# Kernel optimization log

Hardware: AMD Instinct MI355X
Metric: run time of the kernel (lower is better)

## Reference

```python
import jax, jax.numpy as jnp
import numpy as np

K_MASK = -2.3819763e+38
ROPE_THETA = 1000000
MROPE_SECTION = (24, 20, 20)
NORM_EPS = 1e-6


def rms_norm(x, w, eps=NORM_EPS):
    dtype = x.dtype
    x32 = x.astype(jnp.float32)
    rms_inv = jax.lax.rsqrt(jnp.mean(x32 * x32, axis=-1, keepdims=True) + eps)
    return w * (x32 * rms_inv).astype(dtype)


def apply_rope(inputs, positions, head_dim, rope_theta=ROPE_THETA, mrope_section=MROPE_SECTION):
    # positions: [3, B, T] (temporal, height, width); inputs: [B, T, heads, head_dim]
    fraction = 2 * jnp.arange(0, head_dim // 2, dtype=jnp.float32) / head_dim
    timescale = rope_theta ** fraction  # [head_dim//2]
    sinusoid = positions[:, :, :, None].astype(jnp.float32) / timescale  # [3,B,T,hd/2]
    freq = sinusoid[0]
    h_idx = jnp.arange(1, mrope_section[1] * 3, 3)
    w_idx = jnp.arange(2, mrope_section[2] * 3, 3)
    freq = freq.at[..., h_idx].set(sinusoid[1][..., h_idx])
    freq = freq.at[..., w_idx].set(sinusoid[2][..., w_idx])
    freq = freq[:, :, None, :]  # [B,T,1,hd/2]
    sin, cos = jnp.sin(freq), jnp.cos(freq)
    first, second = jnp.split(inputs, 2, axis=-1)
    out = jnp.concatenate([first * cos - second * sin, second * cos + first * sin], axis=-1)
    return out.astype(inputs.dtype)


def setup_inputs() -> dict:
    key = jax.random.key(0)
    ks = jax.random.split(key, 6)
    B, T, D, N, K, H = 2, 1024, 2560, 32, 8, 128
    x = jax.random.normal(ks[0], (B, T, D), dtype=jnp.float32)
    positions = jnp.broadcast_to(jnp.arange(T, dtype=jnp.int32), (3, B, T))
    attn_mask = jnp.tril(jnp.ones((T, T), dtype=bool))[None].repeat(B, axis=0)  # causal [B,T,T]
    wq = jax.random.normal(ks[1], (D, N, H), dtype=jnp.float32) * 0.02
    wk = jax.random.normal(ks[2], (D, K, H), dtype=jnp.float32) * 0.02
    wv = jax.random.normal(ks[3], (D, K, H), dtype=jnp.float32) * 0.02
    wo = jax.random.normal(ks[4], (N, H, D), dtype=jnp.float32) * 0.02
    q_norm_w = jnp.ones((H,), dtype=jnp.float32)
    k_norm_w = jnp.ones((H,), dtype=jnp.float32)
    return {"x": x, "positions": positions, "attn_mask": attn_mask, "wq": wq,
            "wk": wk, "wv": wv, "wo": wo, "q_norm_w": q_norm_w, "k_norm_w": k_norm_w}


def reference(x, positions, attn_mask, wq, wk, wv, wo, q_norm_w, k_norm_w):
    head_dim = wo.shape[1]
    scale = head_dim ** -0.5
    q = rms_norm(jnp.einsum('btd,dnh->btnh', x, wq), q_norm_w)
    k = rms_norm(jnp.einsum('bsd,dkh->bskh', x, wk), k_norm_w)
    v = jnp.einsum('bsd,dkh->bskh', x, wv)
    q = apply_rope(q, positions, head_dim)
    k = apply_rope(k, positions, head_dim)
    b, t, qh, d = q.shape
    _, s, kh, _ = k.shape
    q = q.reshape((b, t, kh, qh // kh, d))  # GQA grouping
    attn = jnp.einsum('bthgd,bshd->bhgts', q, k) * scale
    attn = attn.reshape((b, qh, t, s))
    attn = jnp.where(attn_mask[:, None, :, :], attn, K_MASK)
    attn = jax.nn.softmax(attn.astype(jnp.float32), axis=-1).astype(k.dtype)
    attn = attn.reshape((b, kh, qh // kh, t, s))
    qkv = jnp.einsum('bhgts,bshd->bthgd', attn, v).reshape((b, t, qh, d))
    return jnp.einsum('btnh,nhd->btd', qkv, wo)
```

## Files before the change

kernel.cpp:

```cpp
#include <hip/hip_runtime.h>
#include <hip/hip_bf16.h>

typedef __attribute__((ext_vector_type(8))) __bf16 bf8_t;
typedef __attribute__((ext_vector_type(4))) float f32x4;

#define GLOAD16(gptr, lptr)                                                              \
  __builtin_amdgcn_global_load_lds((const __attribute__((address_space(1))) void*)(gptr), \
                                   (__attribute__((address_space(3))) void*)(lptr), 16, 0, 0)

__device__ __forceinline__ unsigned short f2bf(float f) {
  union { float f; unsigned u; } v; v.f = f;
  return (unsigned short)((v.u + 0x7fffu + ((v.u >> 16) & 1u)) >> 16);
}

__global__ void cast_bf16(const float* __restrict__ in, unsigned short* __restrict__ out, int n4) {
  int i = blockIdx.x * blockDim.x + threadIdx.x;
  if (i >= n4) return;
  float4 v = ((const float4*)in)[i];
  ushort4 o;
  o.x = f2bf(v.x); o.y = f2bf(v.y); o.z = f2bf(v.z); o.w = f2bf(v.w);
  ((ushort4*)out)[i] = o;
}

__global__ void tcast(const float* __restrict__ in, unsigned short* __restrict__ out,
                      int R, int C, int ld, int rowOff) {
  __shared__ float tile[32][33];
  int c0 = blockIdx.x * 32, r0 = blockIdx.y * 32;
  int tx = threadIdx.x, ty = threadIdx.y;
#pragma unroll
  for (int i = 0; i < 4; ++i)
    tile[ty + 8 * i][tx] = in[(size_t)(r0 + ty + 8 * i) * C + c0 + tx];
  __syncthreads();
#pragma unroll
  for (int i = 0; i < 4; ++i)
    out[(size_t)(rowOff + c0 + ty + 8 * i) * ld + r0 + tx] = f2bf(tile[tx][ty + 8 * i]);
}

__global__ __launch_bounds__(512, 2) void gemm256(
    const unsigned short* __restrict__ A,
    const unsigned short* __restrict__ Bt,
    float* __restrict__ C0, float* __restrict__ C1,
    int N, int ldk, int Kslice, int nTileN) {
  __shared__ unsigned short SM[4][2][8192];
  int ks = blockIdx.y;
  float* __restrict__ C = ks ? C1 : C0;
  int kbase = ks * Kslice;
  int bm = blockIdx.x / nTileN, bn = blockIdx.x % nTileN;
  int m0 = bm << 8, n0 = bn << 8;
  int tid = threadIdx.x, lane = tid & 63, w = tid >> 6;
  int wm = w >> 2, wn = w & 3;
  int lrow = lane & 15, lch = lane >> 4;
  int srow = tid >> 2, scol = (tid & 3) << 3;
  int nt = Kslice >> 5;

  f32x4 acc[8][4] = {};

  auto stage = [&](int t) {
    int buf = t & 3;
    int k0 = kbase + (t << 5);
    const unsigned short* Ag = A + (size_t)(m0 + srow) * ldk + k0 + scol;
    const unsigned short* Bg = Bt + (size_t)(n0 + srow) * ldk + k0 + scol;
    unsigned short* Al = &SM[buf][0][w << 9];
    unsigned short* Bl = &SM[buf][1][w << 9];
    GLOAD16(Ag, Al);
    GLOAD16(Ag + (size_t)128 * ldk, Al + 4096);
    GLOAD16(Bg, Bl);
    GLOAD16(Bg + (size_t)128 * ldk, Bl + 4096);
  };

  stage(0);
  stage(1);
  for (int t = 0; t < nt; ++t) {
    if (t + 2 < nt) stage(t + 2);
    if (t + 2 < nt)      asm volatile("s_waitcnt vmcnt(8)" ::: "memory");
    else if (t + 1 < nt) asm volatile("s_waitcnt vmcnt(4)" ::: "memory");
    else                 asm volatile("s_waitcnt vmcnt(0)" ::: "memory");
    asm volatile("s_barrier" ::: "memory");
    int buf = t & 3;
    const unsigned short* As = &SM[buf][0][0];
    const unsigned short* Bs = &SM[buf][1][0];
    bf8_t a[8], b[4];
#pragma unroll
    for (int mi = 0; mi < 8; ++mi)
      a[mi] = *(const bf8_t*)(As + ((wm << 7) + (mi << 4) + lrow) * 32 + (lch << 3));
#pragma unroll
    for (int ni = 0; ni < 4; ++ni)
      b[ni] = *(const bf8_t*)(Bs + ((wn << 6) + (ni << 4) + lrow) * 32 + (lch << 3));
    __builtin_amdgcn_s_setprio(1);
#pragma unroll
    for (int mi = 0; mi < 8; ++mi)
#pragma unroll
      for (int ni = 0; ni < 4; ++ni)
        acc[mi][ni] = __builtin_amdgcn_mfma_f32_16x16x32_bf16(a[mi], b[ni], acc[mi][ni], 0, 0, 0);
    __builtin_amdgcn_s_setprio(0);
  }
  int r0 = m0 + (wm << 7) + (lch << 2);
  int c0 = n0 + (wn << 6) + lrow;
#pragma unroll
  for (int mi = 0; mi < 8; ++mi)
#pragma unroll
    for (int ni = 0; ni < 4; ++ni)
#pragma unroll
      for (int r = 0; r < 4; ++r)
        C[(size_t)(r0 + (mi << 4) + r) * N + c0 + (ni << 4)] = acc[mi][ni][r];
}

__global__ void reduce_add(const float4* __restrict__ a, const float4* __restrict__ b,
                           float4* __restrict__ o, int n4) {
  int i = blockIdx.x * blockDim.x + threadIdx.x;
  if (i >= n4) return;
  float4 x = a[i], y = b[i];
  o[i] = make_float4(x.x + y.x, x.y + y.y, x.z + y.z, x.w + y.w);
}

__global__ __launch_bounds__(128) void normrope(
    const float* __restrict__ qkv, const int* __restrict__ positions,
    const float* __restrict__ qw, const float* __restrict__ kw,
    unsigned short* __restrict__ qb, unsigned short* __restrict__ kb,
    unsigned short* __restrict__ vt) {
  int blk = blockIdx.x;
  int hh = blk % 48, bt = blk / 48;
  int b = bt >> 10, t = bt & 1023;
  int tid = threadIdx.x;
  int colbase = (hh < 32) ? (hh << 7) : ((hh < 40) ? (4096 + ((hh - 32) << 7)) : (5120 + ((hh - 40) << 7)));
  float val = qkv[(size_t)bt * 6144 + colbase + tid];
  if (hh >= 40) {
    vt[((size_t)((b * 8 + hh - 40) * 128 + tid)) * 1024 + t] = f2bf(val);
    return;
  }
  __shared__ float red[2];
  __shared__ float xs[128];
  float ss = val * val;
#pragma unroll
  for (int m = 32; m >= 1; m >>= 1) ss += __shfl_xor(ss, m);
  if ((tid & 63) == 0) red[tid >> 6] = ss;
  __syncthreads();
  float rinv = rsqrtf((red[0] + red[1]) * (1.0f / 128.0f) + 1e-6f);
  float wgt = (hh < 32) ? qw[tid] : kw[tid];
  float xn = val * rinv * wgt;
  xs[tid] = xn;
  __syncthreads();
  float other = xs[tid ^ 64];
  int pos = positions[b * 1024 + t];
  int j = tid & 63;
  float ang = (float)pos * exp2f(-(float)j * 0.31143075889569027f);
  float sv = sinf(ang), cv = cosf(ang);
  float outv = (tid < 64) ? (xn * cv - other * sv) : (xn * cv + other * sv);
  unsigned short o = f2bf(outv);
  if (hh < 32) qb[((size_t)((b * 32 + hh) * 1024 + t)) * 128 + tid] = o;
  else kb[((size_t)((b * 8 + hh - 32) * 1024 + t)) * 128 + tid] = o;
}

__global__ __launch_bounds__(256) void attn(
    const unsigned short* __restrict__ qb,
    const unsigned short* __restrict__ kb,
    const unsigned short* __restrict__ vt,
    unsigned short* __restrict__ ob) {
  __shared__ unsigned short Ks[2][64 * 128];
  __shared__ unsigned short Vs[2][128 * 64];
  __shared__ unsigned short Ps[4][16 * 72];
  int qpair = blockIdx.x, hq = blockIdx.y, b = blockIdx.z;
  int qtA = qpair, qtB = 15 - qpair;
  int kvh = hq >> 2;
  int tid = threadIdx.x, lane = tid & 63, w = tid >> 6;
  int lrow = lane & 15, lko = (lane >> 4) << 3;
  const float scale = 0.08838834764831845f;

  const unsigned short* kbase = kb + ((size_t)(b * 8 + kvh) << 17);
  const unsigned short* vbase = vt + ((size_t)(b * 8 + kvh) << 17);

  int qArow = (qtA << 6) + (w << 4) + lrow;
  int qBrow = (qtB << 6) + (w << 4) + lrow;
  const unsigned short* qpA = qb + ((size_t)((b * 32 + hq) * 1024 + qArow) << 7);
  const unsigned short* qpB = qb + ((size_t)((b * 32 + hq) * 1024 + qBrow) << 7);
  bf8_t qaA[4], qaB[4];
#pragma unroll
  for (int kk = 0; kk < 4; ++kk) {
    qaA[kk] = *(const bf8_t*)(qpA + kk * 32 + lko);
    qaB[kk] = *(const bf8_t*)(qpB + kk * 32 + lko);
  }
  f32x4 accA[8] = {}, accB[8] = {};
  float mA[4], lA[4], mB[4], lB[4];
#pragma unroll
  for (int r = 0; r < 4; ++r) { mA[r] = mB[r] = -3.0e38f; lA[r] = lB[r] = 0.f; }

  int kr_l = lane >> 4, kc_l = lane & 15;
  int vr_l = lane >> 3, vc_l = lane & 7;

  auto stage = [&](int st, int buf) {
    int s0 = st << 6;
    unsigned short* kd = &Ks[buf][0];
    unsigned short* vd = &Vs[buf][0];
#pragma unroll
    for (int i = 0; i < 4; ++i) {
      int si = (w << 2) + i;
      int kr = (si << 2) + kr_l;
      GLOAD16(kbase + (size_t)(s0 + kr) * 128 + ((kc_l ^ (kr & 7)) << 3), kd + (si << 9));
      int vr = (si << 3) + vr_l;
      GLOAD16(vbase + (size_t)vr * 1024 + s0 + ((vc_l ^ (vr & 7)) << 3), vd + (si << 9));
    }
  };

  int qArow0 = (qtA << 6) + (w << 4) + ((lane >> 4) << 2);
  int qBrow0 = (qtB << 6) + (w << 4) + ((lane >> 4) << 2);
  unsigned short* psw = &Ps[w][0];

  auto tilec = [&](int buf, int s0, const bf8_t* qa, f32x4* accO, float* mrun, float* lrun,
                   int qrow0, bool domask) {
    const char* Kb = (const char*)&Ks[buf][0];
    const char* Vb = (const char*)&Vs[buf][0];
    f32x4 sacc[4] = {};
#pragma unroll
    for (int kk = 0; kk < 4; ++kk)
#pragma unroll
      for (int ni = 0; ni < 4; ++ni) {
        int kr = (ni << 4) + lrow;
        const bf8_t* kf = (const bf8_t*)(Kb + kr * 256 + ((((kk << 2) | (lko >> 3)) ^ (kr & 7)) << 4));
        sacc[ni] = __builtin_amdgcn_mfma_f32_16x16x32_bf16(qa[kk], *kf, sacc[ni], 0, 0, 0);
      }
    float p[4][4], rmax[4];
#pragma unroll
    for (int r = 0; r < 4; ++r) rmax[r] = -3.0e38f;
#pragma unroll
    for (int ni = 0; ni < 4; ++ni) {
      int sc = s0 + ni * 16 + lrow;
#pragma unroll
      for (int r = 0; r < 4; ++r) {
        float sv = sacc[ni][r] * scale;
        if (domask) sv = (sc <= qrow0 + r) ? sv : -3.0e38f;
        p[ni][r] = sv;
        rmax[r] = fmaxf(rmax[r], sv);
      }
    }
#pragma unroll
    for (int m = 1; m <= 8; m <<= 1)
#pragma unroll
      for (int r = 0; r < 4; ++r) rmax[r] = fmaxf(rmax[r], __shfl_xor(rmax[r], m));
    float alpha[4], rsum[4];
#pragma unroll
    for (int r = 0; r < 4; ++r) {
      float mn = fmaxf(mrun[r], rmax[r]);
      alpha[r] = __expf(mrun[r] - mn);
      mrun[r] = mn;
      rsum[r] = 0.f;
    }
#pragma unroll
    for (int ni = 0; ni < 4; ++ni)
#pragma unroll
      for (int r = 0; r < 4; ++r) {
        float e = __expf(p[ni][r] - mrun[r]);
        p[ni][r] = e;
        rsum[r] += e;
      }
#pragma unroll
    for (int m = 1; m <= 8; m <<= 1)
#pragma unroll
      for (int r = 0; r < 4; ++r) rsum[r] += __shfl_xor(rsum[r], m);
#pragma unroll
    for (int r = 0; r < 4; ++r) lrun[r] = lrun[r] * alpha[r] + rsum[r];
#pragma unroll
    for (int ni = 0; ni < 8; ++ni)
#pragma unroll
      for (int r = 0; r < 4; ++r) accO[ni][r] *= alpha[r];
#pragma unroll
    for (int ni = 0; ni < 4; ++ni)
#pragma unroll
      for (int r = 0; r < 4; ++r)
        psw[(((lane >> 4) << 2) + r) * 72 + ni * 16 + lrow] = f2bf(p[ni][r]);
    bf8_t pa0 = *(const bf8_t*)(psw + lrow * 72 + lko);
    bf8_t pa1 = *(const bf8_t*)(psw + lrow * 72 + 32 + lko);
#pragma unroll
    for (int ni = 0; ni < 8; ++ni) {
      int vr = (ni << 4) + lrow;
      const bf8_t* v0 = (const bf8_t*)(Vb + vr * 128 + (((lko >> 3) ^ (vr & 7)) << 4));
      const bf8_t* v1 = (const bf8_t*)(Vb + vr * 128 + (((4 | (lko >> 3)) ^ (vr & 7)) << 4));
      accO[ni] = __builtin_amdgcn_mfma_f32_16x16x32_bf16(pa0, *v0, accO[ni], 0, 0, 0);
      accO[ni] = __builtin_amdgcn_mfma_f32_16x16x32_bf16(pa1, *v1, accO[ni], 0, 0, 0);
    }
  };

  stage(0, 0);
  for (int st = 0; st <= qtB; ++st) {
    int buf = st & 1;
    __syncthreads();
    if (st < qtB) stage(st + 1, buf ^ 1);
    if (st <= qtA) tilec(buf, st << 6, qaA, accA, mA, lA, qArow0, st == qtA);
    tilec(buf, st << 6, qaB, accB, mB, lB, qBrow0, st == qtB);
  }

  size_t rowA = (size_t)(b * 1024) + (qtA << 6) + (w << 4) + ((lane >> 4) << 2);
  size_t rowB = (size_t)(b * 1024) + (qtB << 6) + (w << 4) + ((lane >> 4) << 2);
#pragma unroll
  for (int r = 0; r < 4; ++r) {
    float invA = 1.0f / lA[r], invB = 1.0f / lB[r];
#pragma unroll
    for (int ni = 0; ni < 8; ++ni) {
      ob[(rowA + r) * 4096 + hq * 128 + ni * 16 + lrow] = f2bf(accA[ni][r] * invA);
      ob[(rowB + r) * 4096 + hq * 128 + ni * 16 + lrow] = f2bf(accB[ni][r] * invB);
    }
  }
}

extern "C" void kernel_launch(void* const* d_in, const int* in_sizes, int n_in,
                              void* d_out, int out_size, void* d_ws, size_t ws_size,
                              hipStream_t stream) {
  const float* x = (const float*)d_in[0];
  const int* positions = (const int*)d_in[1];
  const float* wq = (const float*)d_in[3];
  const float* wk = (const float*)d_in[4];
  const float* wv = (const float*)d_in[5];
  const float* wo = (const float*)d_in[6];
  const float* qnw = (const float*)d_in[7];
  const float* knw = (const float*)d_in[8];
  float* out = (float*)d_out;

  char* ws = (char*)d_ws;
  unsigned short* x_bf  = (unsigned short*)(ws);
  unsigned short* wqkvT = (unsigned short*)(ws + 10485760);
  unsigned short* woT   = (unsigned short*)(ws + 41943040);
  float*          qkv   = (float*)(ws + 62914560);
  float*          p0    = (float*)(ws + 62914560);
  float*          p1    = (float*)(ws + 83886080);
  unsigned short* q_bf  = (unsigned short*)(ws + 113246208);
  unsigned short* k_bf  = (unsigned short*)(ws + 130023424);
  unsigned short* vt_bf = (unsigned short*)(ws + 134217728);
  unsigned short* a_bf  = (unsigned short*)(ws + 138412032);

  cast_bf16<<<5120, 256, 0, stream>>>(x, x_bf, 2048 * 2560 / 4);
  tcast<<<dim3(128, 80), dim3(32, 8), 0, stream>>>(wq, wqkvT, 2560, 4096, 2560, 0);
  tcast<<<dim3(32, 80), dim3(32, 8), 0, stream>>>(wk, wqkvT, 2560, 1024, 2560, 4096);
  tcast<<<dim3(32, 80), dim3(32, 8), 0, stream>>>(wv, wqkvT, 2560, 1024, 2560, 5120);
  tcast<<<dim3(80, 128), dim3(32, 8), 0, stream>>>(wo, woT, 4096, 2560, 4096, 0);
  gemm256<<<dim3(8 * 24, 1), 512, 0, stream>>>(x_bf, wqkvT, qkv, nullptr, 6144, 2560, 2560, 24);
  normrope<<<2048 * 48, 128, 0, stream>>>(qkv, positions, qnw, knw, q_bf, k_bf, vt_bf);
  attn<<<dim3(8, 32, 2), 256, 0, stream>>>(q_bf, k_bf, vt_bf, a_bf);
  gemm256<<<dim3(8 * 10, 2), 512, 0, stream>>>(a_bf, woT, p0, p1, 2560, 4096, 2048, 10);
  reduce_add<<<5120, 256, 0, stream>>>((const float4*)p0, (const float4*)p1, (float4*)out,
                                       2048 * 2560 / 4);
}
```

Before: 307.6 us.

## Rewrite attention kernel with 32x32 MFMA, 128-row query tiles, register P transpose

```diff
diff --git a/kernel.cpp b/kernel.cpp
--- a/kernel.cpp
+++ b/kernel.cpp
@@ -3,6 +3,7 @@
 
 typedef __attribute__((ext_vector_type(8))) __bf16 bf8_t;
 typedef __attribute__((ext_vector_type(4))) float f32x4;
+typedef __attribute__((ext_vector_type(16))) float f32x16;
 
 #define GLOAD16(gptr, lptr)                                                              \
   __builtin_amdgcn_global_load_lds((const __attribute__((address_space(1))) void*)(gptr), \
@@ -11,6 +12,12 @@
 __device__ __forceinline__ unsigned short f2bf(float f) {
   union { float f; unsigned u; } v; v.f = f;
   return (unsigned short)((v.u + 0x7fffu + ((v.u >> 16) & 1u)) >> 16);
+}
+
+__device__ __forceinline__ unsigned cvtpk_bf16(float a, float b) {
+  unsigned r;
+  asm("v_cvt_pk_bf16_f32 %0, %1, %2" : "=v"(r) : "v"(a), "v"(b));
+  return r;
 }
 
 __global__ void cast_bf16(const float* __restrict__ in, unsigned short* __restrict__ out, int n4) {
@@ -151,153 +158,148 @@
   else kb[((size_t)((b * 8 + hh - 32) * 1024 + t)) * 128 + tid] = o;
 }
 
-__global__ __launch_bounds__(256) void attn(
+__global__ __launch_bounds__(256, 2) void attn(
     const unsigned short* __restrict__ qb,
     const unsigned short* __restrict__ kb,
     const unsigned short* __restrict__ vt,
     unsigned short* __restrict__ ob) {
-  __shared__ unsigned short Ks[2][64 * 128];
-  __shared__ unsigned short Vs[2][128 * 64];
-  __shared__ unsigned short Ps[4][16 * 72];
-  int qpair = blockIdx.x, hq = blockIdx.y, b = blockIdx.z;
-  int qtA = qpair, qtB = 15 - qpair;
+  __shared__ unsigned short Kl[2][64 * 128];
+  __shared__ unsigned short Vl[2][128 * 64];
+  int bx = blockIdx.x, hq = blockIdx.y, b = blockIdx.z;
+  int qt = (bx < 4) ? (7 - bx) : (bx - 4);
   int kvh = hq >> 2;
   int tid = threadIdx.x, lane = tid & 63, w = tid >> 6;
-  int lrow = lane & 15, lko = (lane >> 4) << 3;
-  const float scale = 0.08838834764831845f;
-
+  int qlane = lane & 31, h = lane >> 5;
+  int q0 = (qt << 7) + (w << 5);
+  int qg = q0 + qlane;
   const unsigned short* kbase = kb + ((size_t)(b * 8 + kvh) << 17);
   const unsigned short* vbase = vt + ((size_t)(b * 8 + kvh) << 17);
-
-  int qArow = (qtA << 6) + (w << 4) + lrow;
-  int qBrow = (qtB << 6) + (w << 4) + lrow;
-  const unsigned short* qpA = qb + ((size_t)((b * 32 + hq) * 1024 + qArow) << 7);
-  const unsigned short* qpB = qb + ((size_t)((b * 32 + hq) * 1024 + qBrow) << 7);
-  bf8_t qaA[4], qaB[4];
-#pragma unroll
-  for (int kk = 0; kk < 4; ++kk) {
-    qaA[kk] = *(const bf8_t*)(qpA + kk * 32 + lko);
-    qaB[kk] = *(const bf8_t*)(qpB + kk * 32 + lko);
-  }
-  f32x4 accA[8] = {}, accB[8] = {};
-  float mA[4], lA[4], mB[4], lB[4];
-#pragma unroll
-  for (int r = 0; r < 4; ++r) { mA[r] = mB[r] = -3.0e38f; lA[r] = lB[r] = 0.f; }
-
-  int kr_l = lane >> 4, kc_l = lane & 15;
-  int vr_l = lane >> 3, vc_l = lane & 7;
+  const float c2 = 0.12751744f;
+
+  const unsigned short* qptr = qb + ((size_t)((b * 32 + hq) * 1024 + qg) << 7) + (h << 3);
+  bf8_t qf[8];
+#pragma unroll
+  for (int ds = 0; ds < 8; ++ds) qf[ds] = *(const bf8_t*)(qptr + ds * 16);
+
+  f32x16 o[4] = {};
+  float mrun = -3.0e38f, lrun = 0.f;
+  int last_st = (q0 + 31) >> 6;
+  int nsteps = 2 * qt + 2;
 
   auto stage = [&](int st, int buf) {
     int s0 = st << 6;
-    unsigned short* kd = &Ks[buf][0];
-    unsigned short* vd = &Vs[buf][0];
+    unsigned short* kd = &Kl[buf][0];
+    unsigned short* vd = &Vl[buf][0];
 #pragma unroll
     for (int i = 0; i < 4; ++i) {
-      int si = (w << 2) + i;
-      int kr = (si << 2) + kr_l;
-      GLOAD16(kbase + (size_t)(s0 + kr) * 128 + ((kc_l ^ (kr & 7)) << 3), kd + (si << 9));
-      int vr = (si << 3) + vr_l;
-      GLOAD16(vbase + (size_t)vr * 1024 + s0 + ((vc_l ^ (vr & 7)) << 3), vd + (si << 9));
+      int cid = i * 256 + tid;
+      int kr = cid >> 4, ksl = cid & 15;
+      GLOAD16(kbase + (size_t)(s0 + kr) * 128 + ((ksl ^ (kr & 15)) << 3), kd + cid * 8);
+      int vr = cid >> 3, vsl = cid & 7;
+      GLOAD16(vbase + (size_t)vr * 1024 + s0 + ((vsl ^ (vr & 7)) << 3), vd + cid * 8);
     }
   };
 
-  int qArow0 = (qtA << 6) + (w << 4) + ((lane >> 4) << 2);
-  int qBrow0 = (qtB << 6) + (w << 4) + ((lane >> 4) << 2);
-  unsigned short* psw = &Ps[w][0];
-
-  auto tilec = [&](int buf, int s0, const bf8_t* qa, f32x4* accO, float* mrun, float* lrun,
-                   int qrow0, bool domask) {
-    const char* Kb = (const char*)&Ks[buf][0];
-    const char* Vb = (const char*)&Vs[buf][0];
-    f32x4 sacc[4] = {};
-#pragma unroll
-    for (int kk = 0; kk < 4; ++kk)
-#pragma unroll
-      for (int ni = 0; ni < 4; ++ni) {
-        int kr = (ni << 4) + lrow;
-        const bf8_t* kf = (const bf8_t*)(Kb + kr * 256 + ((((kk << 2) | (lko >> 3)) ^ (kr & 7)) << 4));
-        sacc[ni] = __builtin_amdgcn_mfma_f32_16x16x32_bf16(qa[kk], *kf, sacc[ni], 0, 0, 0);
-      }
-    float p[4][4], rmax[4];
-#pragma unroll
-    for (int r = 0; r < 4; ++r) rmax[r] = -3.0e38f;
-#pragma unroll
-    for (int ni = 0; ni < 4; ++ni) {
-      int sc = s0 + ni * 16 + lrow;
-#pragma unroll
-      for (int r = 0; r < 4; ++r) {
-        float sv = sacc[ni][r] * scale;
-        if (domask) sv = (sc <= qrow0 + r) ? sv : -3.0e38f;
-        p[ni][r] = sv;
-        rmax[r] = fmaxf(rmax[r], sv);
+  stage(0, 0);
+  for (int st = 0; st < nsteps; ++st) {
+    __syncthreads();
+    if (st + 1 < nsteps) stage(st + 1, (st + 1) & 1);
+    if (st <= last_st) {
+      const char* Kb = (const char*)&Kl[st & 1][0];
+      const char* Vb = (const char*)&Vl[st & 1][0];
+      f32x16 s0v = {}, s1v = {};
+#pragma unroll
+      for (int ds = 0; ds < 8; ++ds) {
+        int c = ds * 2 + h;
+        int r0 = qlane, r1 = 32 + qlane;
+        bf8_t k0 = *(const bf8_t*)(Kb + r0 * 256 + ((c ^ (r0 & 15)) << 4));
+        bf8_t k1 = *(const bf8_t*)(Kb + r1 * 256 + ((c ^ (r1 & 15)) << 4));
+        s0v = __builtin_amdgcn_mfma_f32_32x32x16_bf16(k0, qf[ds], s0v, 0, 0, 0);
+        s1v = __builtin_amdgcn_mfma_f32_32x32x16_bf16(k1, qf[ds], s1v, 0, 0, 0);
+      }
+      bool dm = (st == last_st);
+      int kg0 = st << 6;
+      float mt = -3.0e38f;
+#pragma unroll
+      for (int e = 0; e < 16; ++e) {
+        int kl = (e & 3) + 8 * (e >> 2) + 4 * h;
+        if (dm) {
+          if (kg0 + kl > qg) s0v[e] = -3.0e38f;
+          if (kg0 + 32 + kl > qg) s1v[e] = -3.0e38f;
+        }
+        mt = fmaxf(mt, fmaxf(s0v[e], s1v[e]));
+      }
+      mt = fmaxf(mt, __shfl_xor(mt, 32));
+      float mnew = fmaxf(mrun, mt);
+      float alpha = exp2f((mrun - mnew) * c2);
+      float ls = 0.f;
+#pragma unroll
+      for (int e = 0; e < 16; ++e) {
+        s0v[e] = exp2f((s0v[e] - mnew) * c2);
+        s1v[e] = exp2f((s1v[e] - mnew) * c2);
+        ls += s0v[e] + s1v[e];
+      }
+      ls += __shfl_xor(ls, 32);
+      lrun = lrun * alpha + ls;
+      mrun = mnew;
+#pragma unroll
+      for (int db = 0; db < 4; ++db)
+#pragma unroll
+        for (int e = 0; e < 16; ++e) o[db][e] *= alpha;
+      bf8_t pf[4];
+#pragma unroll
+      for (int s = 0; s < 4; ++s) {
+        unsigned w00, w01, w10, w11;
+        {
+          const int B0 = 4 * ((2 * s) & 3);
+          if ((2 * s) >> 2) { w00 = cvtpk_bf16(s1v[B0], s1v[B0 + 1]); w01 = cvtpk_bf16(s1v[B0 + 2], s1v[B0 + 3]); }
+          else              { w00 = cvtpk_bf16(s0v[B0], s0v[B0 + 1]); w01 = cvtpk_bf16(s0v[B0 + 2], s0v[B0 + 3]); }
+        }
+        {
+          const int B1 = 4 * ((2 * s + 1) & 3);
+          if ((2 * s + 1) >> 2) { w10 = cvtpk_bf16(s1v[B1], s1v[B1 + 1]); w11 = cvtpk_bf16(s1v[B1 + 2], s1v[B1 + 3]); }
+          else                  { w10 = cvtpk_bf16(s0v[B1], s0v[B1 + 1]); w11 = cvtpk_bf16(s0v[B1 + 2], s0v[B1 + 3]); }
+        }
+        unsigned sa = h ? w00 : w10, sb = h ? w01 : w11;
+        unsigned ra = __shfl_xor(sa, 32), rb = __shfl_xor(sb, 32);
+        unsigned ka = h ? w10 : w00, kb2 = h ? w11 : w01;
+        unsigned f0 = h ? ra : ka, f1 = h ? rb : kb2;
+        unsigned f2 = h ? ka : ra, f3 = h ? kb2 : rb;
+        uint4 fv = make_uint4(f0, f1, f2, f3);
+        pf[s] = *(bf8_t*)&fv;
+      }
+#pragma unroll
+      for (int db = 0; db < 4; ++db) {
+        int vr = (db << 5) + qlane;
+#pragma unroll
+        for (int s = 0; s < 4; ++s) {
+          int c = (s << 1) + h;
+          bf8_t vf = *(const bf8_t*)(Vb + vr * 128 + ((c ^ (vr & 7)) << 4));
+          o[db] = __builtin_amdgcn_mfma_f32_32x32x16_bf16(vf, pf[s], o[db], 0, 0, 0);
+        }
       }
     }
-#pragma unroll
-    for (int m = 1; m <= 8; m <<= 1)
-#pragma unroll
-      for (int r = 0; r < 4; ++r) rmax[r] = fmaxf(rmax[r], __shfl_xor(rmax[r], m));
-    float alpha[4], rsum[4];
-#pragma unroll
-    for (int r = 0; r < 4; ++r) {
-      float mn = fmaxf(mrun[r], rmax[r]);
-      alpha[r] = __expf(mrun[r] - mn);
-      mrun[r] = mn;
-      rsum[r] = 0.f;
+  }
+
+  __syncthreads();
+  unsigned short* tb = &Kl[0][0] + (w << 12);
+  float inv = 1.0f / lrun;
+#pragma unroll
+  for (int db = 0; db < 4; ++db)
+#pragma unroll
+    for (int rq = 0; rq < 4; ++rq) {
+      int d0 = (db << 5) + (rq << 3) + (h << 2);
+      unsigned lo = ((unsigned)f2bf(o[db][rq * 4 + 1] * inv) << 16) | f2bf(o[db][rq * 4 + 0] * inv);
+      unsigned hi = ((unsigned)f2bf(o[db][rq * 4 + 3] * inv) << 16) | f2bf(o[db][rq * 4 + 2] * inv);
+      *(uint2*)(tb + qlane * 128 + (d0 ^ ((qlane & 15) << 3))) = make_uint2(lo, hi);
     }
-#pragma unroll
-    for (int ni = 0; ni < 4; ++ni)
-#pragma unroll
-      for (int r = 0; r < 4; ++r) {
-        float e = __expf(p[ni][r] - mrun[r]);
-        p[ni][r] = e;
-        rsum[r] += e;
-      }
-#pragma unroll
-    for (int m = 1; m <= 8; m <<= 1)
-#pragma unroll
-      for (int r = 0; r < 4; ++r) rsum[r] += __shfl_xor(rsum[r], m);
-#pragma unroll
-    for (int r = 0; r < 4; ++r) lrun[r] = lrun[r] * alpha[r] + rsum[r];
-#pragma unroll
-    for (int ni = 0; ni < 8; ++ni)
-#pragma unroll
-      for (int r = 0; r < 4; ++r) accO[ni][r] *= alpha[r];
-#pragma unroll
-    for (int ni = 0; ni < 4; ++ni)
-#pragma unroll
-      for (int r = 0; r < 4; ++r)
-        psw[(((lane >> 4) << 2) + r) * 72 + ni * 16 + lrow] = f2bf(p[ni][r]);
-    bf8_t pa0 = *(const bf8_t*)(psw + lrow * 72 + lko);
-    bf8_t pa1 = *(const bf8_t*)(psw + lrow * 72 + 32 + lko);
-#pragma unroll
-    for (int ni = 0; ni < 8; ++ni) {
-      int vr = (ni << 4) + lrow;
-      const bf8_t* v0 = (const bf8_t*)(Vb + vr * 128 + (((lko >> 3) ^ (vr & 7)) << 4));
-      const bf8_t* v1 = (const bf8_t*)(Vb + vr * 128 + (((4 | (lko >> 3)) ^ (vr & 7)) << 4));
-      accO[ni] = __builtin_amdgcn_mfma_f32_16x16x32_bf16(pa0, *v0, accO[ni], 0, 0, 0);
-      accO[ni] = __builtin_amdgcn_mfma_f32_16x16x32_bf16(pa1, *v1, accO[ni], 0, 0, 0);
-    }
-  };
-
-  stage(0, 0);
-  for (int st = 0; st <= qtB; ++st) {
-    int buf = st & 1;
-    __syncthreads();
-    if (st < qtB) stage(st + 1, buf ^ 1);
-    if (st <= qtA) tilec(buf, st << 6, qaA, accA, mA, lA, qArow0, st == qtA);
-    tilec(buf, st << 6, qaB, accB, mB, lB, qBrow0, st == qtB);
-  }
-
-  size_t rowA = (size_t)(b * 1024) + (qtA << 6) + (w << 4) + ((lane >> 4) << 2);
-  size_t rowB = (size_t)(b * 1024) + (qtB << 6) + (w << 4) + ((lane >> 4) << 2);
-#pragma unroll
-  for (int r = 0; r < 4; ++r) {
-    float invA = 1.0f / lA[r], invB = 1.0f / lB[r];
-#pragma unroll
-    for (int ni = 0; ni < 8; ++ni) {
-      ob[(rowA + r) * 4096 + hq * 128 + ni * 16 + lrow] = f2bf(accA[ni][r] * invA);
-      ob[(rowB + r) * 4096 + hq * 128 + ni * 16 + lrow] = f2bf(accB[ni][r] * invB);
-    }
+  int rr = lane >> 1, dh = (lane & 1) << 6;
+  size_t orow = ((size_t)(b * 1024 + q0 + rr) << 12) + (hq << 7);
+#pragma unroll
+  for (int i = 0; i < 8; ++i) {
+    int d8 = dh + i * 8;
+    uint4 vv = *(const uint4*)(tb + rr * 128 + (d8 ^ ((rr & 15) << 3)));
+    *(uint4*)(&ob[orow + d8]) = vv;
   }
 }
 
```

New measurement: 286.1 us. 1.08x faster.
